# Kernel optimization log

Hardware: AMD Instinct MI355X
Metric: run time of the kernel (lower is better)

## Reference

```python
import jax, jax.numpy as jnp
import numpy as np


def _chamfer(xyz1, xyz2):
    # xyz1: [B,N,3], xyz2: [B,M,3]
    sq1 = jnp.sum(xyz1 * xyz1, axis=-1)               # [B,N]
    sq2 = jnp.sum(xyz2 * xyz2, axis=-1)               # [B,M]
    cross = jnp.einsum('bnc,bmc->bnm', xyz1, xyz2)    # [B,N,M]
    d = sq1[:, :, None] + sq2[:, None, :] - 2.0 * cross  # [B,N,M] squared dists
    dist1 = jnp.min(d, axis=2)                        # [B,N]
    idx1 = jnp.argmin(d, axis=2).astype(jnp.int32)    # [B,N]
    dist2 = jnp.min(d, axis=1)                        # [B,M]
    idx2 = jnp.argmin(d, axis=1).astype(jnp.int32)    # [B,M]
    return dist1, dist2, idx1, idx2


def setup_inputs() -> dict:
    key = jax.random.key(0)
    k1, k2 = jax.random.split(key)
    B, N, M = 2, 8192, 8192
    xyz1 = jax.random.normal(k1, (B, N, 3), dtype=jnp.float32)
    xyz2 = jax.random.normal(k2, (B, M, 3), dtype=jnp.float32)
    return {"xyz1": xyz1, "xyz2": xyz2}


def reference(xyz1, xyz2):
    # Matches ChamferDistanceFunction.forward: returns (dist1, dist2, idx1, idx2)
    # with SQUARED distances, as in the CUDA kernel.
    return _chamfer(xyz1, xyz2)
```

## Files before the change

### kernel.cpp

```cpp
#include <hip/hip_runtime.h>
#include <stdint.h>

#define TPB   256
#define Q     4
#define CHUNK 128

typedef unsigned long long ull;

__device__ __forceinline__ uint32_t enc_f32(float f) {
    uint32_t u = __float_as_uint(f);
    return (u & 0x80000000u) ? ~u : (u | 0x80000000u);
}

__device__ __forceinline__ float sq_np(float x, float y, float z) {
    return __fadd_rn(__fadd_rn(__fmul_rn(x, x), __fmul_rn(y, y)), __fmul_rn(z, z));
}

__global__ void __launch_bounds__(TPB) chamfer_pass1(
    const float* __restrict__ xyz1, const float* __restrict__ xyz2,
    ull* __restrict__ P, int B, int N, int M)
{
    __shared__ float4 pts[CHUNK];

    int z   = blockIdx.z;
    int dir = z / B;
    int b   = z - dir * B;

    const float* src; const float* dst; int Ns, Nd; size_t ebase;
    if (dir == 0) { src = xyz1; dst = xyz2; Ns = N; Nd = M; ebase = (size_t)b * N; }
    else          { src = xyz2; dst = xyz1; Ns = M; Nd = N; ebase = (size_t)B * N + (size_t)b * M; }

    int t     = threadIdx.x;
    int mbase = blockIdx.y * CHUNK;

    for (int i = t; i < CHUNK; i += TPB) {
        int m = mbase + i;
        if (m < Nd) {
            const float* p = dst + ((size_t)b * Nd + m) * 3;
            float x = p[0], y = p[1], zz = p[2];
            pts[i] = make_float4(x, y, zz, sq_np(x, y, zz));
        } else {
            pts[i] = make_float4(0.f, 0.f, 0.f, 3.0e38f);
        }
    }

    int n0 = blockIdx.x * (TPB * Q) + t;
    float qx[Q], qy[Q], qz[Q], qs[Q];
    #pragma unroll
    for (int k = 0; k < Q; ++k) {
        int n = n0 + k * TPB;
        if (n < Ns) {
            const float* p = src + ((size_t)b * Ns + n) * 3;
            qx[k] = p[0]; qy[k] = p[1]; qz[k] = p[2];
            qs[k] = sq_np(qx[k], qy[k], qz[k]);
        } else { qx[k] = 0.f; qy[k] = 0.f; qz[k] = 0.f; qs[k] = 0.f; }
    }
    __syncthreads();

    float best[Q];
    int   bidx[Q];
    #pragma unroll
    for (int k = 0; k < Q; ++k) { best[k] = 3.4e38f; bidx[k] = 0; }

    #pragma unroll 4
    for (int i = 0; i < CHUNK; ++i) {
        float4 q = pts[i];
        #pragma unroll
        for (int k = 0; k < Q; ++k) {
            float cross = __fadd_rn(__fadd_rn(__fmul_rn(qx[k], q.x), __fmul_rn(qy[k], q.y)),
                                    __fmul_rn(qz[k], q.z));
            float s = __fadd_rn(qs[k], q.w);
            float d = fmaf(-2.0f, cross, s);
            if (d < best[k]) { best[k] = d; bidx[k] = mbase + i; }
        }
    }

    #pragma unroll
    for (int k = 0; k < Q; ++k) {
        int n = n0 + k * TPB;
        if (n < Ns) {
            ull packed = ((ull)enc_f32(best[k]) << 32) | (unsigned int)bidx[k];
            atomicMin(&P[ebase + n], packed);
        }
    }
}

__global__ void __launch_bounds__(256) chamfer_unpack(
    const ull* __restrict__ P, float* __restrict__ out, int entries)
{
    int e = blockIdx.x * 256 + threadIdx.x;
    if (e < entries) {
        ull pk = P[e];
        uint32_t encu = (uint32_t)(pk >> 32);
        uint32_t idx  = (uint32_t)pk;
        uint32_t bits = (encu & 0x80000000u) ? (encu & 0x7FFFFFFFu) : ~encu;
        out[e]           = __uint_as_float(bits);
        out[entries + e] = (float)idx;
    }
}

__global__ void __launch_bounds__(1024) chamfer_unpack_inplace(float* __restrict__ out)
{
    const int entries = 32768;
    const ull* P = (const ull*)out;
    int t = threadIdx.x;
    ull v[32];
    #pragma unroll
    for (int k = 0; k < 32; ++k) v[k] = P[t + k * 1024];
    __syncthreads();
    #pragma unroll
    for (int k = 0; k < 32; ++k) {
        int e = t + k * 1024;
        ull pk = v[k];
        uint32_t encu = (uint32_t)(pk >> 32);
        uint32_t idx  = (uint32_t)pk;
        uint32_t bits = (encu & 0x80000000u) ? (encu & 0x7FFFFFFFu) : ~encu;
        out[e]           = __uint_as_float(bits);
        out[entries + e] = (float)idx;
    }
}

extern "C" void kernel_launch(void* const* d_in, const int* in_sizes, int n_in,
                              void* d_out, int out_size, void* d_ws, size_t ws_size,
                              hipStream_t stream) {
    const float* xyz1 = (const float*)d_in[0];
    const float* xyz2 = (const float*)d_in[1];
    const int B = 2;
    const int N = in_sizes[0] / (B * 3);
    const int M = in_sizes[1] / (B * 3);

    float* out = (float*)d_out;
    const int entries = B * N + B * M;
    const size_t pbytes = (size_t)entries * sizeof(ull);

    int maxP = (N > M) ? N : M;
    dim3 grid((maxP + TPB * Q - 1) / (TPB * Q), (maxP + CHUNK - 1) / CHUNK, 2 * B);

    if (ws_size >= pbytes) {
        ull* P = (ull*)d_ws;
        hipMemsetAsync(d_ws, 0xFF, pbytes, stream);
        chamfer_pass1<<<grid, TPB, 0, stream>>>(xyz1, xyz2, P, B, N, M);
        chamfer_unpack<<<(entries + 255) / 256, 256, 0, stream>>>(P, out, entries);
    } else {
        ull* P = (ull*)d_out;
        hipMemsetAsync(d_out, 0xFF, pbytes, stream);
        chamfer_pass1<<<grid, TPB, 0, stream>>>(xyz1, xyz2, P, B, N, M);
        if (entries == 32768) {
            chamfer_unpack_inplace<<<1, 1024, 0, stream>>>(out);
        } else {
            chamfer_unpack<<<1, 1, 0, stream>>>((const ull*)d_out, out, 0);
        }
    }
}
```

Before: 111.3 us.

## Replace global atomicMin with per-chunk partial writes and a separate reduction kernel

When the workspace is large enough, each block writes its packed (distance, index) key into a per-chunk slot of a partial buffer instead of doing a 64-bit atomicMin. A new reduce kernel takes the minimum over the 64 chunks per entry and unpacks the result. This removes the memset and atomic contention but adds about 16 MB of partial-buffer traffic plus an extra kernel pass. The in-place fallback now always uses the 1024-thread unpack, which assumes 32768 entries.

```diff
diff --git a/kernel.cpp b/kernel.cpp
--- a/kernel.cpp
+++ b/kernel.cpp
@@ -4,6 +4,7 @@
 #define TPB   256
 #define Q     4
 #define CHUNK 128
+#define NCH   64
 
 typedef unsigned long long ull;
 
@@ -16,9 +17,10 @@
     return __fadd_rn(__fadd_rn(__fmul_rn(x, x), __fmul_rn(y, y)), __fmul_rn(z, z));
 }
 
+template<int MODE>
 __global__ void __launch_bounds__(TPB) chamfer_pass1(
     const float* __restrict__ xyz1, const float* __restrict__ xyz2,
-    ull* __restrict__ P, int B, int N, int M)
+    ull* __restrict__ P, int B, int N, int M, int entries)
 {
     __shared__ float4 pts[CHUNK];
 
@@ -79,10 +81,28 @@
     for (int k = 0; k < Q; ++k) {
         int n = n0 + k * TPB;
         if (n < Ns) {
-            ull packed = ((ull)enc_f32(best[k]) << 32) | (unsigned int)bidx[k];
-            atomicMin(&P[ebase + n], packed);
+            ull key = ((ull)enc_f32(best[k]) << 32) | (unsigned int)bidx[k];
+            if (MODE == 0) P[(size_t)blockIdx.y * entries + ebase + n] = key;
+            else           atomicMin(&P[ebase + n], key);
         }
     }
+}
+
+__global__ void __launch_bounds__(TPB) chamfer_reduce(
+    const ull* __restrict__ P, float* __restrict__ out, int entries)
+{
+    int e = blockIdx.x * TPB + threadIdx.x;
+    if (e >= entries) return;
+    ull best = ~0ull;
+    #pragma unroll 8
+    for (int c = 0; c < NCH; ++c) {
+        ull v = P[(size_t)c * entries + e];
+        if (v < best) best = v;
+    }
+    uint32_t encu = (uint32_t)(best >> 32);
+    uint32_t bits = (encu & 0x80000000u) ? (encu & 0x7FFFFFFFu) : ~encu;
+    out[e]           = __uint_as_float(bits);
+    out[entries + e] = (float)(uint32_t)best;
 }
 
 __global__ void __launch_bounds__(256) chamfer_unpack(
@@ -92,10 +112,9 @@
     if (e < entries) {
         ull pk = P[e];
         uint32_t encu = (uint32_t)(pk >> 32);
-        uint32_t idx  = (uint32_t)pk;
         uint32_t bits = (encu & 0x80000000u) ? (encu & 0x7FFFFFFFu) : ~encu;
         out[e]           = __uint_as_float(bits);
-        out[entries + e] = (float)idx;
+        out[entries + e] = (float)(uint32_t)pk;
     }
 }
 
@@ -113,10 +132,9 @@
         int e = t + k * 1024;
         ull pk = v[k];
         uint32_t encu = (uint32_t)(pk >> 32);
-        uint32_t idx  = (uint32_t)pk;
         uint32_t bits = (encu & 0x80000000u) ? (encu & 0x7FFFFFFFu) : ~encu;
         out[e]           = __uint_as_float(bits);
-        out[entries + e] = (float)idx;
+        out[entries + e] = (float)(uint32_t)pk;
     }
 }
 
@@ -131,24 +149,28 @@
 
     float* out = (float*)d_out;
     const int entries = B * N + B * M;
-    const size_t pbytes = (size_t)entries * sizeof(ull);
+    const int maxP = (N > M) ? N : M;
 
-    int maxP = (N > M) ? N : M;
-    dim3 grid((maxP + TPB * Q - 1) / (TPB * Q), (maxP + CHUNK - 1) / CHUNK, 2 * B);
+    const size_t partBytes = (size_t)NCH * entries * sizeof(ull);
+    const size_t pBytes    = (size_t)entries * sizeof(ull);
 
-    if (ws_size >= pbytes) {
+    dim3 grid((maxP + TPB * Q - 1) / (TPB * Q), NCH, 2 * B);
+
+    if (ws_size >= partBytes && (maxP + CHUNK - 1) / CHUNK <= NCH) {
         ull* P = (ull*)d_ws;
-        hipMemsetAsync(d_ws, 0xFF, pbytes, stream);
-        chamfer_pass1<<<grid, TPB, 0, stream>>>(xyz1, xyz2, P, B, N, M);
+        chamfer_pass1<0><<<grid, TPB, 0, stream>>>(xyz1, xyz2, P, B, N, M, entries);
+        chamfer_reduce<<<(entries + TPB - 1) / TPB, TPB, 0, stream>>>(P, out, entries);
+    } else if (ws_size >= pBytes) {
+        ull* P = (ull*)d_ws;
+        hipMemsetAsync(d_ws, 0xFF, pBytes, stream);
+        dim3 g2((maxP + TPB * Q - 1) / (TPB * Q), (maxP + CHUNK - 1) / CHUNK, 2 * B);
+        chamfer_pass1<1><<<g2, TPB, 0, stream>>>(xyz1, xyz2, P, B, N, M, entries);
         chamfer_unpack<<<(entries + 255) / 256, 256, 0, stream>>>(P, out, entries);
     } else {
         ull* P = (ull*)d_out;
-        hipMemsetAsync(d_out, 0xFF, pbytes, stream);
-        chamfer_pass1<<<grid, TPB, 0, stream>>>(xyz1, xyz2, P, B, N, M);
-        if (entries == 32768) {
-            chamfer_unpack_inplace<<<1, 1024, 0, stream>>>(out);
-        } else {
-            chamfer_unpack<<<1, 1, 0, stream>>>((const ull*)d_out, out, 0);
-        }
+        hipMemsetAsync(d_out, 0xFF, pBytes, stream);
+        dim3 g2((maxP + TPB * Q - 1) / (TPB * Q), (maxP + CHUNK - 1) / CHUNK, 2 * B);
+        chamfer_pass1<1><<<g2, TPB, 0, stream>>>(xyz1, xyz2, P, B, N, M, entries);
+        chamfer_unpack_inplace<<<1, 1024, 0, stream>>>(out);
     }
 }
```

Measured after the change: 119.5 us. 7.4% more time.
